# Performance work log

Hardware: AMD Instinct MI355X
Metric: run time of the kernel (lower is better)

## Reference

```python
import jax, jax.numpy as jnp
import numpy as np
from jax import lax

NUM_CLASSES = 5  # config['training']['num_classes_per_task']
EMBED_DIM = 64


def _conv(x, w, b, pad):
    y = lax.conv_general_dilated(x, w, (1, 1), [(pad, pad), (pad, pad)],
                                 dimension_numbers=('NCHW', 'OIHW', 'NCHW'))
    return y + b[None, :, None, None]


def _maxpool2(x):
    n, c, h, w = x.shape
    return x.reshape(n, c, h // 2, 2, w // 2, 2).max(axis=(3, 5))


def _lenet(x, c1w, c1b, c2w, c2b, f1w, f1b, f2w, f2b, f3w, f3b):
    h = _maxpool2(jax.nn.relu(_conv(x, c1w, c1b, pad=2)))   # [N,6,14,14]
    h = _maxpool2(jax.nn.relu(_conv(h, c2w, c2b, pad=0)))   # [N,16,5,5]
    h = h.reshape(h.shape[0], -1)                            # [N,400]
    h = jax.nn.relu(h @ f1w.T + f1b)                         # [N,120]
    h = jax.nn.relu(h @ f2w.T + f2b)                         # [N,84]
    return h @ f3w.T + f3b                                   # [N,64]


def setup_inputs() -> dict:
    key = jax.random.key(0)
    ks = jax.random.split(key, 12)
    s = 0.1
    return {
        'x': jax.random.normal(ks[0], (20480, 1, 28, 28), dtype=jnp.float32),
        'c1w': jax.random.normal(ks[1], (6, 1, 5, 5), dtype=jnp.float32) * s,
        'c1b': jnp.zeros((6,), dtype=jnp.float32),
        'c2w': jax.random.normal(ks[2], (16, 6, 5, 5), dtype=jnp.float32) * s,
        'c2b': jnp.zeros((16,), dtype=jnp.float32),
        'f1w': jax.random.normal(ks[3], (120, 400), dtype=jnp.float32) * s,
        'f1b': jnp.zeros((120,), dtype=jnp.float32),
        'f2w': jax.random.normal(ks[4], (84, 120), dtype=jnp.float32) * s,
        'f2b': jnp.zeros((84,), dtype=jnp.float32),
        'f3w': jax.random.normal(ks[5], (EMBED_DIM, 84), dtype=jnp.float32) * s,
        'f3b': jnp.zeros((EMBED_DIM,), dtype=jnp.float32),
    }


def reference(x, c1w, c1b, c2w, c2b, f1w, f1b, f2w, f2b, f3w, f3b):
    emb = _lenet(x, c1w, c1b, c2w, c2b, f1w, f1b, f2w, f2b, f3w, f3b)  # [N,D]
    # Source builds a flat prototypes list of all N*D scalars / num_classes,
    # but only indices 0..D-1 are ever read -> first embedding row / num_classes.
    proto = emb[0] / NUM_CLASSES                     # [D]
    s = jax.nn.softmax(emb, axis=1)                  # softmax over dim 1
    # fun_L(x, p) = sqrt((x-p)^2) = |x-p|
    logits = jnp.abs(s - proto[None, :])             # [N,D]
    batch_size = x.shape[0] // NUM_CLASSES
    return logits.reshape(batch_size, NUM_CLASSES, -1)
```

## Files before the change

### kernel.cpp

```cpp
#include <hip/hip_runtime.h>


__device__ __forceinline__ int xcd_swizzle(int orig, int nwg) {
    int xcd = orig & 7, q = nwg >> 3, r = nwg & 7;
    int base = (xcd < r) ? xcd * (q + 1) : r * (q + 1) + (xcd - r) * q;
    return base + (orig >> 3);
}

__global__ __launch_bounds__(256) void transpose_x(
    const float* __restrict__ x, float* __restrict__ xt, int nc)
{
    __shared__ float t[64][65];
    const int tx = threadIdx.x & 63, ty = threadIdx.x >> 6;
    const int p0 = blockIdx.x * 64, n0 = blockIdx.y * 64;
    #pragma unroll
    for (int rr = 0; rr < 16; ++rr) {
        int nl = rr * 4 + ty;
        int pp = p0 + tx;
        int pr = pp >> 5, pc = pp & 31;
        float v = 0.f;
        if (pr >= 2 && pr < 30 && pc >= 2 && pc < 30)
            v = x[(size_t)(n0 + nl) * 784 + (pr - 2) * 28 + (pc - 2)];
        t[tx][nl] = v;
    }
    __syncthreads();
    #pragma unroll
    for (int rr = 0; rr < 16; ++rr) {
        int pl = rr * 4 + ty;
        xt[(size_t)(p0 + pl) * nc + n0 + tx] = t[pl][tx];
    }
}

__global__ __launch_bounds__(256, 2) void conv1_bt(
    const float* __restrict__ xt, const float* __restrict__ c1w,
    const float* __restrict__ c1b, float* __restrict__ p1t, int nc)
{
    const int newid = xcd_swizzle(blockIdx.x, gridDim.x);
    const int grp = newid / 196, pos = newid - grp * 196;
    const int py = pos / 14, px = pos - py * 14;
    const int img = grp * 512 + threadIdx.x * 2;
    const int pbase = (2 * py) * 32 + 2 * px;

    float2 p[36];
    #pragma unroll
    for (int r = 0; r < 6; ++r)
        #pragma unroll
        for (int cc = 0; cc < 6; ++cc)
            p[r * 6 + cc] =
                *(const float2*)&xt[(size_t)(pbase + r * 32 + cc) * nc + img];

    #pragma unroll
    for (int ch = 0; ch < 6; ++ch) {
        float w[25];
        const float* wp = c1w + ch * 25;
        #pragma unroll
        for (int k = 0; k < 25; ++k) w[k] = wp[k];
        float b = c1b[ch];
        float ma = -1e30f, mb = -1e30f;
        #pragma unroll
        for (int dy = 0; dy < 2; ++dy)
        #pragma unroll
        for (int dx = 0; dx < 2; ++dx) {
            float aa = b, ab = b;
            #pragma unroll
            for (int ky = 0; ky < 5; ++ky)
            #pragma unroll
            for (int kx = 0; kx < 5; ++kx) {
                float ww = w[ky * 5 + kx];
                float2 pv = p[(dy + ky) * 6 + dx + kx];
                aa += pv.x * ww;
                ab += pv.y * ww;
            }
            ma = fmaxf(ma, aa); mb = fmaxf(mb, ab);
        }
        float2 o2 = make_float2(fmaxf(ma, 0.f), fmaxf(mb, 0.f));
        *(float2*)&p1t[(size_t)(ch * 196 + pos) * nc + img] = o2;
    }
}

__global__ __launch_bounds__(256, 2) void conv2_bt(
    const float* __restrict__ p1t, const float* __restrict__ c2w,
    const float* __restrict__ c2b, float* __restrict__ ht, int nc)
{
    const int newid = xcd_swizzle(blockIdx.x, gridDim.x);
    const int grp = newid / 25, pos = newid - grp * 25;
    const int qy = pos / 5, qx = pos - qy * 5;
    const int img = grp * 256 + threadIdx.x;
    const int y0 = 2 * qy, x0 = 2 * qx;

    #pragma unroll 1
    for (int pass = 0; pass < 2; ++pass) {
        float acc[32];
        #pragma unroll
        for (int i = 0; i < 32; ++i) acc[i] = 0.f;

        #pragma unroll 1
        for (int ci = 0; ci < 6; ++ci) {
            float pa[36];
            #pragma unroll
            for (int r = 0; r < 6; ++r)
                #pragma unroll
                for (int cc = 0; cc < 6; ++cc)
                    pa[r * 6 + cc] =
                        p1t[(size_t)(ci * 196 + (y0 + r) * 14 + x0 + cc) * nc + img];
            #pragma unroll
            for (int o8 = 0; o8 < 8; ++o8) {
                float w[25];
                const float* wp = c2w + ((pass * 8 + o8) * 6 + ci) * 25;
                #pragma unroll
                for (int k = 0; k < 25; ++k) w[k] = wp[k];
                #pragma unroll
                for (int ky = 0; ky < 5; ++ky)
                #pragma unroll
                for (int kx = 0; kx < 5; ++kx) {
                    float ww = w[ky * 5 + kx];
                    acc[o8*4+0] += pa[ky*6+kx]       * ww;
                    acc[o8*4+1] += pa[ky*6+kx+1]     * ww;
                    acc[o8*4+2] += pa[(ky+1)*6+kx]   * ww;
                    acc[o8*4+3] += pa[(ky+1)*6+kx+1] * ww;
                }
            }
        }
        #pragma unroll
        for (int o8 = 0; o8 < 8; ++o8) {
            int oc = pass * 8 + o8;
            float b = c2b[oc];
            float m = fmaxf(fmaxf(acc[o8*4+0], acc[o8*4+1]),
                            fmaxf(acc[o8*4+2], acc[o8*4+3])) + b;
            ht[(size_t)(oc * 25 + pos) * nc + img] = fmaxf(m, 0.f);
        }
    }
}

__global__ __launch_bounds__(256) void fc1_bt(
    const float* __restrict__ ht, const float* __restrict__ f1w,
    const float* __restrict__ f1b, float* __restrict__ a1t, int nc)
{
    const int newid = xcd_swizzle(blockIdx.x, gridDim.x);
    const int grp = newid / 15, og = newid - grp * 15;
    const int img = grp * 512 + threadIdx.x * 2;
    const float* wb = f1w + og * 8 * 400;

    float2 acc[8];
    #pragma unroll
    for (int j = 0; j < 8; ++j) acc[j] = make_float2(0.f, 0.f);

    #pragma unroll 4
    for (int k = 0; k < 400; ++k) {
        float2 hv = *(const float2*)&ht[(size_t)k * nc + img];
        #pragma unroll
        for (int j = 0; j < 8; ++j) {
            float w = wb[j * 400 + k];
            acc[j].x += hv.x * w;
            acc[j].y += hv.y * w;
        }
    }
    #pragma unroll
    for (int j = 0; j < 8; ++j) {
        int o = og * 8 + j;
        float b = f1b[o];
        float2 o2 = make_float2(fmaxf(acc[j].x + b, 0.f),
                                fmaxf(acc[j].y + b, 0.f));
        *(float2*)&a1t[(size_t)o * nc + img] = o2;
    }
}

__global__ __launch_bounds__(256) void fc2_bt(
    const float* __restrict__ a1t, const float* __restrict__ f2w,
    const float* __restrict__ f2b, float* __restrict__ a2t, int nc)
{
    const int newid = xcd_swizzle(blockIdx.x, gridDim.x);
    const int grp = newid / 12, og = newid - grp * 12;
    const int img = grp * 512 + threadIdx.x * 2;
    const float* wb = f2w + og * 7 * 120;

    float2 acc[7];
    #pragma unroll
    for (int j = 0; j < 7; ++j) acc[j] = make_float2(0.f, 0.f);

    #pragma unroll 4
    for (int k = 0; k < 120; ++k) {
        float2 hv = *(const float2*)&a1t[(size_t)k * nc + img];
        #pragma unroll
        for (int j = 0; j < 7; ++j) {
            float w = wb[j * 120 + k];
            acc[j].x += hv.x * w;
            acc[j].y += hv.y * w;
        }
    }
    #pragma unroll
    for (int j = 0; j < 7; ++j) {
        int o = og * 7 + j;
        float b = f2b[o];
        float2 o2 = make_float2(fmaxf(acc[j].x + b, 0.f),
                                fmaxf(acc[j].y + b, 0.f));
        *(float2*)&a2t[(size_t)o * nc + img] = o2;
    }
}

__global__ __launch_bounds__(256) void fc3_bt(
    const float* __restrict__ a2t, const float* __restrict__ f3w,
    const float* __restrict__ f3b, float* __restrict__ embt,
    int nc, int Ntot, int n0)
{
    const int newid = xcd_swizzle(blockIdx.x, gridDim.x);
    const int grp = newid / 8, og = newid - grp * 8;
    const int limg = grp * 512 + threadIdx.x * 2;
    const float* wb = f3w + og * 8 * 84;

    float2 acc[8];
    #pragma unroll
    for (int j = 0; j < 8; ++j) acc[j] = make_float2(0.f, 0.f);

    #pragma unroll 4
    for (int k = 0; k < 84; ++k) {
        float2 hv = *(const float2*)&a2t[(size_t)k * nc + limg];
        #pragma unroll
        for (int j = 0; j < 8; ++j) {
            float w = wb[j * 84 + k];
            acc[j].x += hv.x * w;
            acc[j].y += hv.y * w;
        }
    }
    #pragma unroll
    for (int j = 0; j < 8; ++j) {
        int o = og * 8 + j;
        float b = f3b[o];
        float2 o2 = make_float2(acc[j].x + b, acc[j].y + b);
        *(float2*)&embt[(size_t)o * Ntot + n0 + limg] = o2;
    }
}

__global__ __launch_bounds__(256) void proto_head_t(
    const float* __restrict__ embt, float* __restrict__ out, int N)
{
    const int img = blockIdx.x * 256 + threadIdx.x;
    float v[64];
    float m = -1e30f;
    #pragma unroll
    for (int o = 0; o < 64; ++o) {
        v[o] = embt[(size_t)o * N + img];
        m = fmaxf(m, v[o]);
    }
    float s = 0.f;
    #pragma unroll
    for (int o = 0; o < 64; ++o) {
        v[o] = __expf(v[o] - m);
        s += v[o];
    }
    float inv = __frcp_rn(s);
    #pragma unroll
    for (int o = 0; o < 64; o += 4) {
        float4 r;
        r.x = fabsf(v[o+0] * inv - embt[(size_t)(o+0) * N] * 0.2f);
        r.y = fabsf(v[o+1] * inv - embt[(size_t)(o+1) * N] * 0.2f);
        r.z = fabsf(v[o+2] * inv - embt[(size_t)(o+2) * N] * 0.2f);
        r.w = fabsf(v[o+3] * inv - embt[(size_t)(o+3) * N] * 0.2f);
        *(float4*)&out[(size_t)img * 64 + o] = r;
    }
}

extern "C" void kernel_launch(void* const* d_in, const int* in_sizes, int n_in,
                              void* d_out, int out_size, void* d_ws, size_t ws_size,
                              hipStream_t stream)
{
    const float* x   = (const float*)d_in[0];
    const float* c1w = (const float*)d_in[1];
    const float* c1b = (const float*)d_in[2];
    const float* c2w = (const float*)d_in[3];
    const float* c2b = (const float*)d_in[4];
    const float* f1w = (const float*)d_in[5];
    const float* f1b = (const float*)d_in[6];
    const float* f2w = (const float*)d_in[7];
    const float* f2b = (const float*)d_in[8];
    const float* f3w = (const float*)d_in[9];
    const float* f3b = (const float*)d_in[10];
    float* out = (float*)d_out;

    const int N = in_sizes[0] / 784;
    float* base = (float*)d_ws;

    int c = 40;
    const int cands[] = {1, 2, 4, 5, 8, 10, 20, 40};
    for (int k = 0; k < 8; ++k) {
        int cd = cands[k];
        if (N % cd) continue;
        int ncq = N / cd;
        if (ncq % 512) continue;
        size_t need = (size_t)8800 * ncq + (size_t)256 * N;
        if (need <= ws_size) { c = cd; break; }
    }
    const int nc = N / c;

    float* xt   = base;
    float* p1t  = base + (size_t)1024 * nc;
    float* ht_  = base;
    float* a1t  = p1t;
    float* a2t  = p1t + (size_t)120 * nc;
    float* embt = base + (size_t)2200 * nc;

    for (int k = 0; k < c; ++k) {
        int n0 = k * nc;
        transpose_x<<<dim3(16, nc / 64), 256, 0, stream>>>(
            x + (size_t)n0 * 784, xt, nc);
        conv1_bt<<<196 * (nc / 512), 256, 0, stream>>>(
            xt, c1w, c1b, p1t, nc);
        conv2_bt<<<25 * (nc / 256), 256, 0, stream>>>(
            p1t, c2w, c2b, ht_, nc);
        fc1_bt<<<15 * (nc / 512), 256, 0, stream>>>(
            ht_, f1w, f1b, a1t, nc);
        fc2_bt<<<12 * (nc / 512), 256, 0, stream>>>(
            a1t, f2w, f2b, a2t, nc);
        fc3_bt<<<8 * (nc / 512), 256, 0, stream>>>(
            a2t, f3w, f3b, embt, nc, N, n0);
    }
    proto_head_t<<<N / 256, 256, 0, stream>>>(embt, out, N);
}
```

Measured before the change: 297.3 us.

## Stream conv input rows and compute all output channels in one pass

```diff
diff --git a/kernel.cpp b/kernel.cpp
--- a/kernel.cpp
+++ b/kernel.cpp
@@ -39,41 +39,51 @@
     const int grp = newid / 196, pos = newid - grp * 196;
     const int py = pos / 14, px = pos - py * 14;
     const int img = grp * 512 + threadIdx.x * 2;
-    const int pbase = (2 * py) * 32 + 2 * px;
-
-    float2 p[36];
-    #pragma unroll
-    for (int r = 0; r < 6; ++r)
+    const float* pb = xt + (size_t)((2 * py) * 32 + 2 * px) * nc + img;
+
+    float2 acc[24];
+    #pragma unroll
+    for (int i = 0; i < 24; ++i) acc[i] = make_float2(0.f, 0.f);
+
+    #pragma unroll
+    for (int r = 0; r < 6; ++r) {
+        float2 row[6];
         #pragma unroll
         for (int cc = 0; cc < 6; ++cc)
-            p[r * 6 + cc] =
-                *(const float2*)&xt[(size_t)(pbase + r * 32 + cc) * nc + img];
-
+            row[cc] = *(const float2*)&pb[(size_t)(r * 32 + cc) * nc];
+        #pragma unroll
+        for (int ch = 0; ch < 6; ++ch) {
+            const float* wp = c1w + ch * 25;
+            if (r <= 4) {
+                #pragma unroll
+                for (int kx = 0; kx < 5; ++kx) {
+                    float w = wp[r * 5 + kx];
+                    acc[ch*4+0].x += row[kx].x   * w;
+                    acc[ch*4+0].y += row[kx].y   * w;
+                    acc[ch*4+1].x += row[kx+1].x * w;
+                    acc[ch*4+1].y += row[kx+1].y * w;
+                }
+            }
+            if (r >= 1) {
+                #pragma unroll
+                for (int kx = 0; kx < 5; ++kx) {
+                    float w = wp[(r - 1) * 5 + kx];
+                    acc[ch*4+2].x += row[kx].x   * w;
+                    acc[ch*4+2].y += row[kx].y   * w;
+                    acc[ch*4+3].x += row[kx+1].x * w;
+                    acc[ch*4+3].y += row[kx+1].y * w;
+                }
+            }
+        }
+    }
     #pragma unroll
     for (int ch = 0; ch < 6; ++ch) {
-        float w[25];
-        const float* wp = c1w + ch * 25;
-        #pragma unroll
-        for (int k = 0; k < 25; ++k) w[k] = wp[k];
         float b = c1b[ch];
-        float ma = -1e30f, mb = -1e30f;
-        #pragma unroll
-        for (int dy = 0; dy < 2; ++dy)
-        #pragma unroll
-        for (int dx = 0; dx < 2; ++dx) {
-            float aa = b, ab = b;
-            #pragma unroll
-            for (int ky = 0; ky < 5; ++ky)
-            #pragma unroll
-            for (int kx = 0; kx < 5; ++kx) {
-                float ww = w[ky * 5 + kx];
-                float2 pv = p[(dy + ky) * 6 + dx + kx];
-                aa += pv.x * ww;
-                ab += pv.y * ww;
-            }
-            ma = fmaxf(ma, aa); mb = fmaxf(mb, ab);
-        }
-        float2 o2 = make_float2(fmaxf(ma, 0.f), fmaxf(mb, 0.f));
+        float mx = fmaxf(fmaxf(acc[ch*4+0].x, acc[ch*4+1].x),
+                         fmaxf(acc[ch*4+2].x, acc[ch*4+3].x)) + b;
+        float my = fmaxf(fmaxf(acc[ch*4+0].y, acc[ch*4+1].y),
+                         fmaxf(acc[ch*4+2].y, acc[ch*4+3].y)) + b;
+        float2 o2 = make_float2(fmaxf(mx, 0.f), fmaxf(my, 0.f));
         *(float2*)&p1t[(size_t)(ch * 196 + pos) * nc + img] = o2;
     }
 }
@@ -88,47 +98,47 @@
     const int img = grp * 256 + threadIdx.x;
     const int y0 = 2 * qy, x0 = 2 * qx;
 
+    float acc[64];
+    #pragma unroll
+    for (int i = 0; i < 64; ++i) acc[i] = 0.f;
+
     #pragma unroll 1
-    for (int pass = 0; pass < 2; ++pass) {
-        float acc[32];
-        #pragma unroll
-        for (int i = 0; i < 32; ++i) acc[i] = 0.f;
-
-        #pragma unroll 1
-        for (int ci = 0; ci < 6; ++ci) {
-            float pa[36];
+    for (int ci = 0; ci < 6; ++ci) {
+        const float* pb = p1t + (size_t)(ci * 196 + y0 * 14 + x0) * nc + img;
+        #pragma unroll
+        for (int r = 0; r < 6; ++r) {
+            float row[6];
             #pragma unroll
-            for (int r = 0; r < 6; ++r)
-                #pragma unroll
-                for (int cc = 0; cc < 6; ++cc)
-                    pa[r * 6 + cc] =
-                        p1t[(size_t)(ci * 196 + (y0 + r) * 14 + x0 + cc) * nc + img];
+            for (int cc = 0; cc < 6; ++cc)
+                row[cc] = pb[(size_t)(r * 14 + cc) * nc];
             #pragma unroll
-            for (int o8 = 0; o8 < 8; ++o8) {
-                float w[25];
-                const float* wp = c2w + ((pass * 8 + o8) * 6 + ci) * 25;
-                #pragma unroll
-                for (int k = 0; k < 25; ++k) w[k] = wp[k];
-                #pragma unroll
-                for (int ky = 0; ky < 5; ++ky)
-                #pragma unroll
-                for (int kx = 0; kx < 5; ++kx) {
-                    float ww = w[ky * 5 + kx];
-                    acc[o8*4+0] += pa[ky*6+kx]       * ww;
-                    acc[o8*4+1] += pa[ky*6+kx+1]     * ww;
-                    acc[o8*4+2] += pa[(ky+1)*6+kx]   * ww;
-                    acc[o8*4+3] += pa[(ky+1)*6+kx+1] * ww;
+            for (int oc = 0; oc < 16; ++oc) {
+                const float* wp = c2w + (oc * 6 + ci) * 25;
+                if (r <= 4) {
+                    #pragma unroll
+                    for (int kx = 0; kx < 5; ++kx) {
+                        float w = wp[r * 5 + kx];
+                        acc[oc*4+0] += row[kx]   * w;
+                        acc[oc*4+1] += row[kx+1] * w;
+                    }
+                }
+                if (r >= 1) {
+                    #pragma unroll
+                    for (int kx = 0; kx < 5; ++kx) {
+                        float w = wp[(r - 1) * 5 + kx];
+                        acc[oc*4+2] += row[kx]   * w;
+                        acc[oc*4+3] += row[kx+1] * w;
+                    }
                 }
             }
         }
-        #pragma unroll
-        for (int o8 = 0; o8 < 8; ++o8) {
-            int oc = pass * 8 + o8;
-            float b = c2b[oc];
-            float m = fmaxf(fmaxf(acc[o8*4+0], acc[o8*4+1]),
-                            fmaxf(acc[o8*4+2], acc[o8*4+3])) + b;
-            ht[(size_t)(oc * 25 + pos) * nc + img] = fmaxf(m, 0.f);
-        }
+    }
+    #pragma unroll
+    for (int oc = 0; oc < 16; ++oc) {
+        float b = c2b[oc];
+        float m = fmaxf(fmaxf(acc[oc*4+0], acc[oc*4+1]),
+                        fmaxf(acc[oc*4+2], acc[oc*4+3])) + b;
+        ht[(size_t)(oc * 25 + pos) * nc + img] = fmaxf(m, 0.f);
     }
 }
 
```

New measurement: 296.0 us. Within noise of the previous version (-0.4%).
